# Kernel tuning notes

Hardware: AMD Instinct MI355X
Metric: run time of the kernel (lower is better)

The kernel has to match this reference:

```python
import jax, jax.numpy as jnp
import numpy as np

H = 8  # n_head
EPS = 1e-5


def layernorm(x, g, b):
    m = jnp.mean(x, -1, keepdims=True)
    v = jnp.mean((x - m) ** 2, -1, keepdims=True)
    return (x - m) * jax.lax.rsqrt(v + EPS) * g + b


def setup_inputs() -> dict:
    key = jax.random.key(0)
    ks = jax.random.split(key, 32)
    b, t, d, f, n_mem, l_mem = 4, 256, 512, 2048, 64, 128
    sd = 1.0 / np.sqrt(d)
    sf = 1.0 / np.sqrt(f)
    rn = lambda k, shape, s: jax.random.normal(k, shape, jnp.float32) * s
    inp = {
        'dec_output': rn(ks[0], (b, t, d), 1.0),
        'tgt_mask': jnp.ones((b, t), dtype=bool),
        'mem_attn_out': rn(ks[1], (b, t, n_mem + 1), 1.0),
        'enc_out_mem': rn(ks[2], (n_mem, l_mem, d), 1.0),
        'tgt_emb_mem': rn(ks[3], (n_mem, l_mem, d), 1.0),
        'tgt_mask_mem': jnp.ones((n_mem, l_mem), dtype=bool),
        # MultiHeadedAttention params
        'Wq': rn(ks[4], (d, d), sd), 'bq': jnp.zeros((d,)),
        'Wk': rn(ks[5], (d, d), sd), 'bk': jnp.zeros((d,)),
        'Wv': rn(ks[6], (d, d), sd), 'bv': jnp.zeros((d,)),
        'Wo': rn(ks[7], (d, d), sd), 'bo': jnp.zeros((d,)),
        # LayerNorms (norms[0] pre, norms[1] post)
        'g0': jnp.ones((d,)), 'be0': jnp.zeros((d,)),
        'g1': jnp.ones((d,)), 'be1': jnp.zeros((d,)),
        # pos_ffn (applied to attended tokens)
        'W1': rn(ks[8], (d, f), sd), 'bf1': jnp.zeros((f,)),
        'W2': rn(ks[9], (f, d), sf), 'bf2': jnp.zeros((d,)),
        # pos_ffn2 (applied to all tokens at the end)
        'W3': rn(ks[10], (d, f), sd), 'bf3': jnp.zeros((f,)),
        'W4': rn(ks[11], (f, d), sf), 'bf4': jnp.zeros((d,)),
    }
    return inp


def reference(dec_output, tgt_mask, mem_attn_out, enc_out_mem, tgt_emb_mem, tgt_mask_mem,
              Wq, bq, Wk, bk, Wv, bv, Wo, bo, g0, be0, g1, be1,
              W1, bf1, W2, bf2, W3, bf3, W4, bf4):
    b, t, d = dec_output.shape
    dh = d // H
    x = layernorm(dec_output, g0, be0)                       # norms[0]

    samples = jnp.argmax(mem_attn_out, -1) - 1               # [b,t], -1 => no memory
    valid = samples >= 0
    s = jnp.clip(samples, 0, None)                           # safe gather index

    # Per-token gather of the selected memory entry (irregular access).
    K = enc_out_mem[s]                                       # [b,t,l_mem,d]
    V = tgt_emb_mem[s]                                       # [b,t,l_mem,d]
    kmask = tgt_mask_mem[s]                                  # [b,t,l_mem] True=valid

    # Single-row attention: token (b,t) queries memory entry samples[b,t].
    q = (x @ Wq + bq).reshape(b, t, H, dh)
    k = (K @ Wk + bk).reshape(b, t, -1, H, dh)
    v = (V @ Wv + bv).reshape(b, t, -1, H, dh)
    scores = jnp.einsum('bthd,btlhd->bthl', q, k) / np.sqrt(dh)
    scores = jnp.where(kmask[:, :, None, :], scores, -1e9)
    attn = jax.nn.softmax(scores, axis=-1)
    ctx = jnp.einsum('bthl,btlhd->bthd', attn, v).reshape(b, t, d)
    st = ctx @ Wo + bo + x                                   # residual = query

    # pos_ffn (residual) then norms[1]
    st = st + jax.nn.relu(st @ W1 + bf1) @ W2 + bf2
    st = layernorm(st, g1, be1)

    # scatter-back: zero for tokens with sample == -1
    x = x + jnp.where(valid[..., None], st, 0.0)

    # pos_ffn2 (residual)
    out = x + jax.nn.relu(x @ W3 + bf3) @ W4 + bf4
    return out
```

## Files before the change

kernel.cpp:

```cpp
#include <hip/hip_runtime.h>
#include <hip/hip_bf16.h>
#include <math.h>

#define DD    512
#define FF    2048
#define NMEM  64
#define LMEM  128
#define NH    8
#define DH    64
#define NTOK  1024
#define NMROW 8192

typedef __attribute__((ext_vector_type(4))) float f32x4;
typedef __attribute__((ext_vector_type(8))) short bf16x8;

__device__ inline unsigned short f2b(float f) {
    union { float f; unsigned int i; } u; u.f = f;
    unsigned int r = u.i + 0x7FFFu + ((u.i >> 16) & 1u);
    return (unsigned short)(r >> 16);
}
__device__ inline float b2f(unsigned short b) {
    union { unsigned int i; float f; } u; u.i = ((unsigned int)b) << 16;
    return u.f;
}
__device__ __forceinline__ void gload_lds(const void* src, void* dst) {
    __builtin_amdgcn_global_load_lds((const __attribute__((address_space(1))) void*)src,
        (__attribute__((address_space(3))) void*)dst, 16, 0, 0);
}

struct WSeg { const float* src; unsigned short* dst; int K, N, tile0; };
struct PrepArgs {
    const float4 *enc, *emb; ushort4 *encb, *embb;
    WSeg s[8];
    const float *mem_attn;
    int *samples, *blist, *bstart;
    const float *dec, *g0, *be0;
    float *x; unsigned short *xb, *ctxb;
};

__global__ __launch_bounds__(256)
void prep_kernel(PrepArgs a) {
    __shared__ float ld[32][33];
    __shared__ float red[8];
    __shared__ int ibuf[64 + 65 + 64];
    int b = blockIdx.x, tid = threadIdx.x;
    if (b < 4096) {
        int i = b * 256 + tid;
        float4 va = a.enc[i];
        a.encb[i] = make_ushort4(f2b(va.x), f2b(va.y), f2b(va.z), f2b(va.w));
        float4 vb = a.emb[i];
        a.embb[i] = make_ushort4(f2b(vb.x), f2b(vb.y), f2b(vb.z), f2b(vb.w));
        return;
    }
    if (b < 9216) {
        int t = b - 4096;
        int si = 0;
#pragma unroll
        for (int i = 1; i < 8; ++i) if (t >= a.s[i].tile0) si = i;
        const float* src = a.s[si].src;
        unsigned short* dst = a.s[si].dst;
        int K = a.s[si].K, N = a.s[si].N;
        int lt = t - a.s[si].tile0;
        int ntn = N >> 5;
        int k0 = (lt / ntn) << 5, n0 = (lt % ntn) << 5;
        int r = tid >> 3, c = (tid & 7) << 2;
        float4 v = *(const float4*)(src + (size_t)(k0 + r) * N + n0 + c);
        ld[r][c] = v.x; ld[r][c + 1] = v.y; ld[r][c + 2] = v.z; ld[r][c + 3] = v.w;
        __syncthreads();
        ushort4 o = make_ushort4(f2b(ld[c][r]), f2b(ld[c + 1][r]),
                                 f2b(ld[c + 2][r]), f2b(ld[c + 3][r]));
        *(ushort4*)(dst + (size_t)(n0 + r) * K + k0 + c) = o;
        return;
    }
    if (b < 10240) {
        int row = b - 9216;
        const float* xr = a.dec + (size_t)row * DD;
        float v0 = xr[tid], v1 = xr[tid + 256];
        float s = v0 + v1, s2 = v0 * v0 + v1 * v1;
        for (int off = 32; off > 0; off >>= 1) {
            s  += __shfl_down(s,  off, 64);
            s2 += __shfl_down(s2, off, 64);
        }
        int wave = tid >> 6, lane = tid & 63;
        if (lane == 0) { red[wave] = s; red[4 + wave] = s2; }
        __syncthreads();
        float S  = red[0] + red[1] + red[2] + red[3];
        float S2 = red[4] + red[5] + red[6] + red[7];
        float mean = S / (float)DD;
        float inv  = rsqrtf(S2 / (float)DD - mean * mean + 1e-5f);
        float o0 = (v0 - mean) * inv * a.g0[tid]       + a.be0[tid];
        float o1 = (v1 - mean) * inv * a.g0[tid + 256] + a.be0[tid + 256];
        size_t base = (size_t)row * DD;
        a.x[base + tid] = o0; a.x[base + tid + 256] = o1;
        a.xb[base + tid] = f2b(o0); a.xb[base + tid + 256] = f2b(o1);
        ((unsigned*)a.ctxb)[row * 256 + tid] = 0u;
        return;
    }
    int* scnt  = ibuf;
    int* soff  = ibuf + 64;
    int* scnt2 = ibuf + 129;
    if (tid < 64) { scnt[tid] = 0; scnt2[tid] = 0; }
    __syncthreads();
    int mys[4];
#pragma unroll
    for (int k = 0; k < 4; ++k) {
        int t = k * 256 + tid;
        const float* r = a.mem_attn + (size_t)t * (NMEM + 1);
        float best = r[0]; int bi = 0;
        for (int i = 1; i < NMEM + 1; ++i) {
            float v = r[i];
            if (v > best) { best = v; bi = i; }
        }
        int s = bi - 1;
        a.samples[t] = s; mys[k] = s;
        if (s >= 0) atomicAdd(&scnt[s], 1);
    }
    __syncthreads();
    if (tid == 0) {
        int run = 0;
        for (int e = 0; e < 64; ++e) { soff[e] = run; run += scnt[e]; }
        soff[64] = run;
    }
    __syncthreads();
    if (tid < 65) a.bstart[tid] = soff[tid];
#pragma unroll
    for (int k = 0; k < 4; ++k) {
        int t = k * 256 + tid;
        int s = mys[k];
        if (s >= 0) {
            int pos = soff[s] + atomicAdd(&scnt2[s], 1);
            a.blist[pos] = t;
        }
    }
}

__global__ __launch_bounds__(256)
void ln_scatter_kernel(const float* __restrict__ st2, const float* __restrict__ g,
                       const float* __restrict__ be, const float* __restrict__ x,
                       const int* __restrict__ samples, float* __restrict__ x2,
                       unsigned short* __restrict__ x2b) {
    int row = blockIdx.x;
    const float* xr = st2 + (size_t)row * DD;
    int tid = threadIdx.x;
    float v0 = xr[tid], v1 = xr[tid + 256];
    float s = v0 + v1, s2 = v0 * v0 + v1 * v1;
    for (int off = 32; off > 0; off >>= 1) {
        s  += __shfl_down(s,  off, 64);
        s2 += __shfl_down(s2, off, 64);
    }
    __shared__ float red[8];
    int wave = tid >> 6, lane = tid & 63;
    if (lane == 0) { red[wave] = s; red[4 + wave] = s2; }
    __syncthreads();
    float S  = red[0] + red[1] + red[2] + red[3];
    float S2 = red[4] + red[5] + red[6] + red[7];
    float mean = S / (float)DD;
    float inv  = rsqrtf(S2 / (float)DD - mean * mean + 1e-5f);
    float valid = (samples[row] >= 0) ? 1.f : 0.f;
    size_t base = (size_t)row * DD;
    float l0 = (v0 - mean) * inv * g[tid]       + be[tid];
    float l1 = (v1 - mean) * inv * g[tid + 256] + be[tid + 256];
    float r0 = x[base + tid]       + valid * l0;
    float r1 = x[base + tid + 256] + valid * l1;
    x2[base + tid] = r0; x2[base + tid + 256] = r1;
    x2b[base + tid] = f2b(r0); x2b[base + tid + 256] = f2b(r1);
}

template<int MI, int NI, int BK>
__device__ __forceinline__
void gemm_core(const unsigned short* __restrict__ A, const unsigned short* __restrict__ Bt,
               const float* __restrict__ bias, const float* __restrict__ res,
               float* __restrict__ C, unsigned short* __restrict__ Cb,
               int N, int K, int relu, int bx, int by,
               unsigned short* As0, unsigned short* As1,
               unsigned short* Bs0, unsigned short* Bs1) {
    constexpr int BM = MI * 32, BN = NI * 32;
    constexpr int CPR = BK / 8;
    constexpr int RB  = BK * 2;
    const int tid = threadIdx.x;
    const int lane = tid & 63, w = tid >> 6;
    const int wm = (w >> 1) * (MI * 16), wn = (w & 1) * (NI * 16);
    const int m0 = by * BM, n0 = bx * BN;
    f32x4 acc[MI][NI] = {};

    auto stage = [&](unsigned short* As, unsigned short* Bs, int k0) {
#pragma unroll
        for (int it = 0; it < BM * CPR / 256; ++it) {
            int f = it * 256 + tid;
            int row = f / CPR, ch = f % CPR;
            int sch = ch ^ (row & 7);
            gload_lds((const char*)(A + (size_t)(m0 + row) * K + k0) + sch * 16,
                      (char*)As + f * 16);
        }
#pragma unroll
        for (int it = 0; it < BN * CPR / 256; ++it) {
            int f = it * 256 + tid;
            int row = f / CPR, ch = f % CPR;
            int sch = ch ^ (row & 7);
            gload_lds((const char*)(Bt + (size_t)(n0 + row) * K + k0) + sch * 16,
                      (char*)Bs + f * 16);
        }
    };

    const int nt = K / BK;
    stage(As0, Bs0, 0);
    __syncthreads();
    for (int t = 0; t < nt; ++t) {
        unsigned short* As = (t & 1) ? As1 : As0;
        unsigned short* Bs = (t & 1) ? Bs1 : Bs0;
        if (t + 1 < nt) stage((t & 1) ? As0 : As1, (t & 1) ? Bs0 : Bs1, (t + 1) * BK);
#pragma unroll
        for (int kk = 0; kk < BK / 32; ++kk) {
            bf16x8 af[MI], bfr[NI];
#pragma unroll
            for (int mi = 0; mi < MI; ++mi) {
                int row = wm + mi * 16 + (lane & 15);
                int ch = kk * 4 + (lane >> 4);
                af[mi] = *(const bf16x8*)((const char*)As + row * RB + ((ch ^ (row & 7)) * 16));
            }
#pragma unroll
            for (int ni = 0; ni < NI; ++ni) {
                int row = wn + ni * 16 + (lane & 15);
                int ch = kk * 4 + (lane >> 4);
                bfr[ni] = *(const bf16x8*)((const char*)Bs + row * RB + ((ch ^ (row & 7)) * 16));
            }
#pragma unroll
            for (int mi = 0; mi < MI; ++mi)
#pragma unroll
                for (int ni = 0; ni < NI; ++ni)
                    acc[mi][ni] = __builtin_amdgcn_mfma_f32_16x16x32_bf16(af[mi], bfr[ni], acc[mi][ni], 0, 0, 0);
        }
        __syncthreads();
    }
#pragma unroll
    for (int mi = 0; mi < MI; ++mi) {
#pragma unroll
        for (int ni = 0; ni < NI; ++ni) {
            int col = n0 + wn + ni * 16 + (lane & 15);
            float bv = bias[col];
#pragma unroll
            for (int j = 0; j < 4; ++j) {
                int row = m0 + wm + mi * 16 + (lane >> 4) * 4 + j;
                size_t idx = (size_t)row * N + col;
                float v = acc[mi][ni][j] + bv;
                if (res)  v += res[idx];
                if (relu) v = fmaxf(v, 0.f);
                if (C)  C[idx] = v;
                if (Cb) Cb[idx] = f2b(v);
            }
        }
    }
}

template<int MI, int NI, int BK, int RELU>
__global__ __launch_bounds__(256)
void gemm_kernel(const unsigned short* __restrict__ A, const unsigned short* __restrict__ Bt,
                 const float* __restrict__ bias, const float* __restrict__ res,
                 float* __restrict__ C, unsigned short* __restrict__ Cb, int N, int K) {
    __shared__ __align__(16) unsigned short As0[MI * 32 * BK], As1[MI * 32 * BK];
    __shared__ __align__(16) unsigned short Bs0[NI * 32 * BK], Bs1[NI * 32 * BK];
    gemm_core<MI, NI, BK>(A, Bt, bias, res, C, Cb, N, K, RELU, blockIdx.x, blockIdx.y,
                          As0, As1, Bs0, Bs1);
}

__global__ __launch_bounds__(256)
void attn_fused_kernel(const unsigned short* __restrict__ encb,
                       const unsigned short* __restrict__ embb,
                       const unsigned short* __restrict__ xb,
                       const unsigned short* __restrict__ WkT,
                       const unsigned short* __restrict__ WvT,
                       const unsigned short* __restrict__ WqT,
                       const float* __restrict__ bk, const float* __restrict__ bv,
                       const float* __restrict__ bq,
                       const int* __restrict__ blist, const int* __restrict__ bstart,
                       unsigned short* __restrict__ ctxb) {
    __shared__ __align__(16) unsigned short As[128 * 64];
    __shared__ __align__(16) unsigned short Ws[64 * 64];
    __shared__ __align__(16) unsigned short Ks[128 * 64];
    __shared__ __align__(16) unsigned short Vt[64 * 128];
    __shared__ float qsb[32 * 64];
    __shared__ float ps[2][128];
    __shared__ float red[8];
    __shared__ int toks[32];
    const int b = blockIdx.x, e = b & 63, h = b >> 6, tid = threadIdx.x;
    const int lane = tid & 63, w = tid >> 6;
    const int beg = bstart[e], end = bstart[e + 1];
    if (end <= beg) return;

#pragma unroll 1
    for (int ph = 0; ph < 2; ++ph) {
        const unsigned short* Am = (ph ? embb : encb) + (size_t)e * LMEM * DD;
        const unsigned short* Wm = (ph ? WvT : WkT) + (size_t)h * DH * DD;
        const float* bias = ph ? bv : bk;
        f32x4 acc[2][4] = {};
        for (int k0 = 0; k0 < DD; k0 += 64) {
            __syncthreads();
#pragma unroll
            for (int it = 0; it < 4; ++it) {
                int f = it * 256 + tid;
                int row = f >> 3, ch = f & 7, sch = ch ^ (row & 7);
                gload_lds((const char*)(Am + (size_t)row * DD + k0) + sch * 16,
                          (char*)As + f * 16);
            }
#pragma unroll
            for (int it = 0; it < 2; ++it) {
                int f = it * 256 + tid;
                int row = f >> 3, ch = f & 7, sch = ch ^ (row & 7);
                gload_lds((const char*)(Wm + (size_t)row * DD + k0) + sch * 16,
                          (char*)Ws + f * 16);
            }
            __syncthreads();
#pragma unroll
            for (int kk = 0; kk < 2; ++kk) {
                int ch = kk * 4 + (lane >> 4);
                bf16x8 af[2], bfr[4];
#pragma unroll
                for (int mi = 0; mi < 2; ++mi) {
                    int row = w * 32 + mi * 16 + (lane & 15);
                    af[mi] = *(const bf16x8*)((const char*)As + row * 128 + ((ch ^ (row & 7)) * 16));
                }
#pragma unroll
                for (int ni = 0; ni < 4; ++ni) {
                    int row = ni * 16 + (lane & 15);
                    bfr[ni] = *(const bf16x8*)((const char*)Ws + row * 128 + ((ch ^ (row & 7)) * 16));
                }
#pragma unroll
                for (int mi = 0; mi < 2; ++mi)
#pragma unroll
                    for (int ni = 0; ni < 4; ++ni)
                        acc[mi][ni] = __builtin_amdgcn_mfma_f32_16x16x32_bf16(af[mi], bfr[ni], acc[mi][ni], 0, 0, 0);
            }
        }
#pragma unroll
        for (int mi = 0; mi < 2; ++mi) {
#pragma unroll
            for (int ni = 0; ni < 4; ++ni) {
                int d = ni * 16 + (lane & 15);
                float bvv = bias[h * DH + d];
#pragma unroll
                for (int j = 0; j < 4; ++j) {
                    int l = w * 32 + mi * 16 + (lane >> 4) * 4 + j;
                    unsigned short val = f2b(acc[mi][ni][j] + bvv);
                    if (ph == 0) {
                        int c = d >> 3;
                        *(unsigned short*)((char*)Ks + l * 128 + ((c ^ (l & 7)) * 16) + (d & 7) * 2) = val;
                    } else {
                        int cc = l >> 3;
                        int slot = (cc & 8) | ((cc ^ d) & 7);
                        *(unsigned short*)((char*)Vt + d * 256 + slot * 16 + (l & 7) * 2) = val;
                    }
                }
            }
        }
    }

    const int sub = tid >> 7, lt = tid & 127;
    for (int g0 = beg; g0 < end; g0 += 32) {
        int gcnt = end - g0; if (gcnt > 32) gcnt = 32;
        __syncthreads();
        if (tid < 32) toks[tid] = blist[(g0 + tid < end) ? (g0 + tid) : (end - 1)];
        f32x4 qacc[2] = {};
        for (int k0 = 0; k0 < DD; k0 += 64) {
            __syncthreads();
            {
                int row = tid >> 3, ch = tid & 7, sch = ch ^ (row & 7);
                gload_lds((const char*)(xb + (size_t)toks[row] * DD + k0) + sch * 16,
                          (char*)As + tid * 16);
            }
#pragma unroll
            for (int it = 0; it < 2; ++it) {
                int f = it * 256 + tid;
                int row = f >> 3, ch = f & 7, sch = ch ^ (row & 7);
                gload_lds((const char*)(WqT + (size_t)(h * DH + row) * DD + k0) + sch * 16,
                          (char*)Ws + f * 16);
            }
            __syncthreads();
#pragma unroll
            for (int kk = 0; kk < 2; ++kk) {
                int ch = kk * 4 + (lane >> 4);
                int ar = (w >> 1) * 16 + (lane & 15);
                bf16x8 af = *(const bf16x8*)((const char*)As + ar * 128 + ((ch ^ (ar & 7)) * 16));
#pragma unroll
                for (int ni = 0; ni < 2; ++ni) {
                    int br = (w & 1) * 32 + ni * 16 + (lane & 15);
                    bf16x8 bfr = *(const bf16x8*)((const char*)Ws + br * 128 + ((ch ^ (br & 7)) * 16));
                    qacc[ni] = __builtin_amdgcn_mfma_f32_16x16x32_bf16(af, bfr, qacc[ni], 0, 0, 0);
                }
            }
        }
#pragma unroll
        for (int ni = 0; ni < 2; ++ni)
#pragma unroll
            for (int j = 0; j < 4; ++j) {
                int r = (w >> 1) * 16 + (lane >> 4) * 4 + j;
                int d = (w & 1) * 32 + ni * 16 + (lane & 15);
                qsb[r * 64 + d] = qacc[ni][j] + bq[h * DH + d];
            }
        __syncthreads();

        int iters = (gcnt + 1) >> 1;
        for (int it = 0; it < iters; ++it) {
            int tl = it * 2 + sub;
            float sc = 0.f;
#pragma unroll
            for (int c = 0; c < 8; ++c) {
                bf16x8 kv = *(const bf16x8*)((char*)Ks + lt * 128 + ((c ^ (lt & 7)) * 16));
#pragma unroll
                for (int j = 0; j < 8; ++j) sc = fmaf(qsb[tl * 64 + c * 8 + j], b2f((unsigned short)kv[j]), sc);
            }
            sc *= 0.125f;
            float mx = sc;
            for (int off = 32; off > 0; off >>= 1) mx = fmaxf(mx, __shfl_xor(mx, off, 64));
            if ((tid & 63) == 0) red[tid >> 6] = mx;
            __syncthreads();
            mx = fmaxf(red[sub * 2], red[sub * 2 + 1]);
            float ex = __expf(sc - mx);
            float sm = ex;
            for (int off = 32; off > 0; off >>= 1) sm += __shfl_xor(sm, off, 64);
            if ((tid & 63) == 0) red[4 + (tid >> 6)] = sm;
            __syncthreads();
            sm = red[4 + sub * 2] + red[4 + sub * 2 + 1];
            ps[sub][lt] = ex / sm;
            __syncthreads();
            if (tid < 128) {
                int sub2 = tid >> 6, d = tid & 63;
                int tl2 = it * 2 + sub2;
                if (g0 + tl2 < end) {
                    int tok2 = toks[tl2];
                    float acc2 = 0.f;
#pragma unroll
                    for (int cc = 0; cc < 16; ++cc) {
                        int slot = (cc & 8) | ((cc ^ d) & 7);
                        bf16x8 vv = *(const bf16x8*)((char*)Vt + d * 256 + slot * 16);
#pragma unroll
                        for (int j = 0; j < 8; ++j) acc2 = fmaf(ps[sub2][cc * 8 + j], b2f((unsigned short)vv[j]), acc2);
                    }
                    ctxb[(size_t)tok2 * DD + h * DH + d] = f2b(acc2);
                }
            }
            __syncthreads();
        }
    }
}

extern "C" void kernel_launch(void* const* d_in, const int* in_sizes, int n_in,
                              void* d_out, int out_size, void* d_ws, size_t ws_size,
                              hipStream_t stream) {
    const float* dec      = (const float*)d_in[0];
    const float* mem_attn = (const float*)d_in[2];
    const float* enc_mem  = (const float*)d_in[3];
    const float* emb_mem  = (const float*)d_in[4];
    const float* Wq = (const float*)d_in[6];  const float* bq = (const float*)d_in[7];
    const float* Wk = (const float*)d_in[8];  const float* bk = (const float*)d_in[9];
    const float* Wv = (const float*)d_in[10]; const float* bv = (const float*)d_in[11];
    const float* Wo = (const float*)d_in[12]; const float* bo = (const float*)d_in[13];
    const float* g0 = (const float*)d_in[14]; const float* be0 = (const float*)d_in[15];
    const float* g1 = (const float*)d_in[16]; const float* be1 = (const float*)d_in[17];
    const float* W1 = (const float*)d_in[18]; const float* bf1 = (const float*)d_in[19];
    const float* W2 = (const float*)d_in[20]; const float* bf2 = (const float*)d_in[21];
    const float* W3 = (const float*)d_in[22]; const float* bf3 = (const float*)d_in[23];
    const float* W4 = (const float*)d_in[24]; const float* bf4 = (const float*)d_in[25];
    float* out = (float*)d_out;

    const size_t MB = 1u << 20;
    char* ws = (char*)d_ws;
    unsigned short* encb  = (unsigned short*)(ws + 0 * MB);
    unsigned short* embb  = (unsigned short*)(ws + 8 * MB);
    unsigned short* WqT = (unsigned short*)(ws + 32 * MB);
    unsigned short* WkT = (unsigned short*)(ws + 32 * MB + 512 * 1024);
    unsigned short* WvT = (unsigned short*)(ws + 33 * MB);
    unsigned short* WoT = (unsigned short*)(ws + 33 * MB + 512 * 1024);
    unsigned short* W1T = (unsigned short*)(ws + 34 * MB);
    unsigned short* W2T = (unsigned short*)(ws + 36 * MB);
    unsigned short* W3T = (unsigned short*)(ws + 38 * MB);
    unsigned short* W4T = (unsigned short*)(ws + 40 * MB);
    float*          x    = (float*)(ws + 42 * MB);
    unsigned short* xb   = (unsigned short*)(ws + 44 * MB);
    unsigned short* ctxb = (unsigned short*)(ws + 47 * MB);
    int*         samples = (int*)(ws + 48 * MB);
    int*         blist   = (int*)(ws + 48 * MB + 4096);
    int*         bstart  = (int*)(ws + 48 * MB + 8192);
    float*          st   = (float*)(ws + 0 * MB);
    unsigned short* stb  = (unsigned short*)(ws + 2 * MB);
    unsigned short* h1b  = (unsigned short*)(ws + 3 * MB);
    float*          st2  = (float*)(ws + 8 * MB);
    float*          x2   = (float*)(ws + 10 * MB);
    unsigned short* x2b  = (unsigned short*)(ws + 12 * MB);
    unsigned short* h2b  = (unsigned short*)(ws + 13 * MB);

    PrepArgs pa;
    pa.enc = (const float4*)enc_mem; pa.emb = (const float4*)emb_mem;
    pa.encb = (ushort4*)encb; pa.embb = (ushort4*)embb;
    pa.s[0] = { Wq, WqT, DD, DD,    0 };
    pa.s[1] = { Wk, WkT, DD, DD,  256 };
    pa.s[2] = { Wv, WvT, DD, DD,  512 };
    pa.s[3] = { Wo, WoT, DD, DD,  768 };
    pa.s[4] = { W1, W1T, DD, FF, 1024 };
    pa.s[5] = { W2, W2T, FF, DD, 2048 };
    pa.s[6] = { W3, W3T, DD, FF, 3072 };
    pa.s[7] = { W4, W4T, FF, DD, 4096 };
    pa.mem_attn = mem_attn; pa.samples = samples; pa.blist = blist; pa.bstart = bstart;
    pa.dec = dec; pa.g0 = g0; pa.be0 = be0;
    pa.x = x; pa.xb = xb; pa.ctxb = ctxb;
    prep_kernel<<<10241, 256, 0, stream>>>(pa);
    attn_fused_kernel<<<512, 256, 0, stream>>>(encb, embb, xb, WkT, WvT, WqT,
                                               bk, bv, bq, blist, bstart, ctxb);
    gemm_kernel<1,1,128,0><<<dim3(16, 32), 256, 0, stream>>>(ctxb, WoT, bo, x, st, stb, DD, DD);
    gemm_kernel<2,2,128,1><<<dim3(32, 16), 256, 0, stream>>>(stb, W1T, bf1, nullptr, nullptr, h1b, FF, DD);
    gemm_kernel<1,1,128,0><<<dim3(16, 32), 256, 0, stream>>>(h1b, W2T, bf2, st, st2, nullptr, DD, FF);
    ln_scatter_kernel<<<NTOK, 256, 0, stream>>>(st2, g1, be1, x, samples, x2, x2b);
    gemm_kernel<2,2,128,1><<<dim3(32, 16), 256, 0, stream>>>(x2b, W3T, bf3, nullptr, nullptr, h2b, FF, DD);
    gemm_kernel<1,1,128,0><<<dim3(16, 32), 256, 0, stream>>>(h2b, W4T, bf4, x2, out, nullptr, DD, FF);
}
```

Measured before the change: 122.6 us.

## Double-buffer attention projections, warp-local softmax, and retune GEMM K tiles

The fused attention kernel now stages its K/V and Q projection loads in double-buffered 32-wide K slices, so the next slice loads while the current one is multiplied. It also gives each wavefront its own token for scores, softmax and context, using readlane broadcasts, which removes block-wide barriers and shared reduction buffers. The Wo GEMM becomes a single-stage kernel with K=512 in one tile, and the W2/W4 GEMMs use BK=256. The cost is more synchronisation steps in the projection loops and larger shared-memory use in the retuned GEMMs, which may lower occupancy.

```diff
diff --git a/kernel.cpp b/kernel.cpp
--- a/kernel.cpp
+++ b/kernel.cpp
@@ -263,24 +263,33 @@
                           As0, As1, Bs0, Bs1);
 }
 
+template<int MI, int NI, int BK, int RELU>
 __global__ __launch_bounds__(256)
-void attn_fused_kernel(const unsigned short* __restrict__ encb,
-                       const unsigned short* __restrict__ embb,
-                       const unsigned short* __restrict__ xb,
-                       const unsigned short* __restrict__ WkT,
-                       const unsigned short* __restrict__ WvT,
-                       const unsigned short* __restrict__ WqT,
-                       const float* __restrict__ bk, const float* __restrict__ bv,
-                       const float* __restrict__ bq,
-                       const int* __restrict__ blist, const int* __restrict__ bstart,
-                       unsigned short* __restrict__ ctxb) {
-    __shared__ __align__(16) unsigned short As[128 * 64];
-    __shared__ __align__(16) unsigned short Ws[64 * 64];
+void gemm1_kernel(const unsigned short* __restrict__ A, const unsigned short* __restrict__ Bt,
+                  const float* __restrict__ bias, const float* __restrict__ res,
+                  float* __restrict__ C, unsigned short* __restrict__ Cb, int N) {
+    __shared__ __align__(16) unsigned short As[MI * 32 * BK];
+    __shared__ __align__(16) unsigned short Bs[NI * 32 * BK];
+    gemm_core<MI, NI, BK>(A, Bt, bias, res, C, Cb, N, BK, RELU, blockIdx.x, blockIdx.y,
+                          As, As, Bs, Bs);
+}
+
+__global__ __launch_bounds__(256)
+void attn_fused2_kernel(const unsigned short* __restrict__ encb,
+                        const unsigned short* __restrict__ embb,
+                        const unsigned short* __restrict__ xb,
+                        const unsigned short* __restrict__ WkT,
+                        const unsigned short* __restrict__ WvT,
+                        const unsigned short* __restrict__ WqT,
+                        const float* __restrict__ bk, const float* __restrict__ bv,
+                        const float* __restrict__ bq,
+                        const int* __restrict__ blist, const int* __restrict__ bstart,
+                        unsigned short* __restrict__ ctxb) {
+    __shared__ __align__(16) unsigned short As0[128 * 32], As1[128 * 32];
+    __shared__ __align__(16) unsigned short Ws0[64 * 32],  Ws1[64 * 32];
     __shared__ __align__(16) unsigned short Ks[128 * 64];
     __shared__ __align__(16) unsigned short Vt[64 * 128];
     __shared__ float qsb[32 * 64];
-    __shared__ float ps[2][128];
-    __shared__ float red[8];
     __shared__ int toks[32];
     const int b = blockIdx.x, e = b & 63, h = b >> 6, tid = threadIdx.x;
     const int lane = tid & 63, w = tid >> 6;
@@ -289,47 +298,43 @@
 
 #pragma unroll 1
     for (int ph = 0; ph < 2; ++ph) {
-        const unsigned short* Am = (ph ? embb : encb) + (size_t)e * LMEM * DD;
-        const unsigned short* Wm = (ph ? WvT : WkT) + (size_t)h * DH * DD;
+        const unsigned short* Am = (ph ? embb : encb) + (size_t)e * (LMEM * DD);
+        const unsigned short* Wm = (ph ? WvT : WkT) + (size_t)h * (DH * DD);
         const float* bias = ph ? bv : bk;
         f32x4 acc[2][4] = {};
-        for (int k0 = 0; k0 < DD; k0 += 64) {
+        auto stageP = [&](unsigned short* As, unsigned short* Ws, int k0) {
+#pragma unroll
+            for (int it = 0; it < 2; ++it) {
+                int f = it * 256 + tid, row = f >> 2, ch = f & 3, s = ch ^ (row & 3);
+                gload_lds((const char*)(Am + (size_t)row * DD + k0) + s * 16, (char*)As + f * 16);
+            }
+            { int f = tid, row = f >> 2, ch = f & 3, s = ch ^ (row & 3);
+              gload_lds((const char*)(Wm + (size_t)row * DD + k0) + s * 16, (char*)Ws + f * 16); }
+        };
+        stageP(As0, Ws0, 0);
+        __syncthreads();
+        for (int t = 0; t < 16; ++t) {
+            unsigned short* As = (t & 1) ? As1 : As0;
+            unsigned short* Ws = (t & 1) ? Ws1 : Ws0;
+            if (t + 1 < 16) stageP((t & 1) ? As0 : As1, (t & 1) ? Ws0 : Ws1, (t + 1) * 32);
+            int ch = lane >> 4;
+            bf16x8 af[2], bfr[4];
+#pragma unroll
+            for (int mi = 0; mi < 2; ++mi) {
+                int row = w * 32 + mi * 16 + (lane & 15);
+                af[mi] = *(const bf16x8*)((const char*)As + row * 64 + ((ch ^ (row & 3)) * 16));
+            }
+#pragma unroll
+            for (int ni = 0; ni < 4; ++ni) {
+                int row = ni * 16 + (lane & 15);
+                bfr[ni] = *(const bf16x8*)((const char*)Ws + row * 64 + ((ch ^ (row & 3)) * 16));
+            }
+#pragma unroll
+            for (int mi = 0; mi < 2; ++mi)
+#pragma unroll
+                for (int ni = 0; ni < 4; ++ni)
+                    acc[mi][ni] = __builtin_amdgcn_mfma_f32_16x16x32_bf16(af[mi], bfr[ni], acc[mi][ni], 0, 0, 0);
             __syncthreads();
-#pragma unroll
-            for (int it = 0; it < 4; ++it) {
-                int f = it * 256 + tid;
-                int row = f >> 3, ch = f & 7, sch = ch ^ (row & 7);
-                gload_lds((const char*)(Am + (size_t)row * DD + k0) + sch * 16,
-                          (char*)As + f * 16);
-            }
-#pragma unroll
-            for (int it = 0; it < 2; ++it) {
-                int f = it * 256 + tid;
-                int row = f >> 3, ch = f & 7, sch = ch ^ (row & 7);
-                gload_lds((const char*)(Wm + (size_t)row * DD + k0) + sch * 16,
-                          (char*)Ws + f * 16);
-            }
-            __syncthreads();
-#pragma unroll
-            for (int kk = 0; kk < 2; ++kk) {
-                int ch = kk * 4 + (lane >> 4);
-                bf16x8 af[2], bfr[4];
-#pragma unroll
-                for (int mi = 0; mi < 2; ++mi) {
-                    int row = w * 32 + mi * 16 + (lane & 15);
-                    af[mi] = *(const bf16x8*)((const char*)As + row * 128 + ((ch ^ (row & 7)) * 16));
-                }
-#pragma unroll
-                for (int ni = 0; ni < 4; ++ni) {
-                    int row = ni * 16 + (lane & 15);
-                    bfr[ni] = *(const bf16x8*)((const char*)Ws + row * 128 + ((ch ^ (row & 7)) * 16));
-                }
-#pragma unroll
-                for (int mi = 0; mi < 2; ++mi)
-#pragma unroll
-                    for (int ni = 0; ni < 4; ++ni)
-                        acc[mi][ni] = __builtin_amdgcn_mfma_f32_16x16x32_bf16(af[mi], bfr[ni], acc[mi][ni], 0, 0, 0);
-            }
         }
 #pragma unroll
         for (int mi = 0; mi < 2; ++mi) {
@@ -354,39 +359,38 @@
         }
     }
 
-    const int sub = tid >> 7, lt = tid & 127;
     for (int g0 = beg; g0 < end; g0 += 32) {
         int gcnt = end - g0; if (gcnt > 32) gcnt = 32;
         __syncthreads();
         if (tid < 32) toks[tid] = blist[(g0 + tid < end) ? (g0 + tid) : (end - 1)];
+        __syncthreads();
         f32x4 qacc[2] = {};
-        for (int k0 = 0; k0 < DD; k0 += 64) {
+        auto stageQ = [&](unsigned short* As, unsigned short* Ws, int k0) {
+            if (tid < 128) {
+                int row = tid >> 2, ch = tid & 3, s = ch ^ (row & 3);
+                gload_lds((const char*)(xb + (size_t)toks[row] * DD + k0) + s * 16,
+                          (char*)As + tid * 16);
+            }
+            { int f = tid, row = f >> 2, ch = f & 3, s = ch ^ (row & 3);
+              gload_lds((const char*)(WqT + (size_t)(h * DH + row) * DD + k0) + s * 16,
+                        (char*)Ws + f * 16); }
+        };
+        stageQ(As0, Ws0, 0);
+        __syncthreads();
+        for (int t = 0; t < 16; ++t) {
+            unsigned short* As = (t & 1) ? As1 : As0;
+            unsigned short* Ws = (t & 1) ? Ws1 : Ws0;
+            if (t + 1 < 16) stageQ((t & 1) ? As0 : As1, (t & 1) ? Ws0 : Ws1, (t + 1) * 32);
+            int ch = lane >> 4;
+            int ar = (w >> 1) * 16 + (lane & 15);
+            bf16x8 af = *(const bf16x8*)((const char*)As + ar * 64 + ((ch ^ (ar & 3)) * 16));
+#pragma unroll
+            for (int ni = 0; ni < 2; ++ni) {
+                int br = (w & 1) * 32 + ni * 16 + (lane & 15);
+                bf16x8 bfr = *(const bf16x8*)((const char*)Ws + br * 64 + ((ch ^ (br & 3)) * 16));
+                qacc[ni] = __builtin_amdgcn_mfma_f32_16x16x32_bf16(af, bfr, qacc[ni], 0, 0, 0);
+            }
             __syncthreads();
-            {
-                int row = tid >> 3, ch = tid & 7, sch = ch ^ (row & 7);
-                gload_lds((const char*)(xb + (size_t)toks[row] * DD + k0) + sch * 16,
-                          (char*)As + tid * 16);
-            }
-#pragma unroll
-            for (int it = 0; it < 2; ++it) {
-                int f = it * 256 + tid;
-                int row = f >> 3, ch = f & 7, sch = ch ^ (row & 7);
-                gload_lds((const char*)(WqT + (size_t)(h * DH + row) * DD + k0) + sch * 16,
-                          (char*)Ws + f * 16);
-            }
-            __syncthreads();
-#pragma unroll
-            for (int kk = 0; kk < 2; ++kk) {
-                int ch = kk * 4 + (lane >> 4);
-                int ar = (w >> 1) * 16 + (lane & 15);
-                bf16x8 af = *(const bf16x8*)((const char*)As + ar * 128 + ((ch ^ (ar & 7)) * 16));
-#pragma unroll
-                for (int ni = 0; ni < 2; ++ni) {
-                    int br = (w & 1) * 32 + ni * 16 + (lane & 15);
-                    bf16x8 bfr = *(const bf16x8*)((const char*)Ws + br * 128 + ((ch ^ (br & 7)) * 16));
-                    qacc[ni] = __builtin_amdgcn_mfma_f32_16x16x32_bf16(af, bfr, qacc[ni], 0, 0, 0);
-                }
-            }
         }
 #pragma unroll
         for (int ni = 0; ni < 2; ++ni)
@@ -398,47 +402,44 @@
             }
         __syncthreads();
 
-        int iters = (gcnt + 1) >> 1;
-        for (int it = 0; it < iters; ++it) {
-            int tl = it * 2 + sub;
-            float sc = 0.f;
+        for (int tl = w; tl < gcnt; tl += 4) {
+            int token = toks[tl];
+            float qv = qsb[tl * 64 + lane];
+            int qb = __float_as_int(qv);
+            float sc0 = 0.f, sc1 = 0.f;
 #pragma unroll
             for (int c = 0; c < 8; ++c) {
-                bf16x8 kv = *(const bf16x8*)((char*)Ks + lt * 128 + ((c ^ (lt & 7)) * 16));
-#pragma unroll
-                for (int j = 0; j < 8; ++j) sc = fmaf(qsb[tl * 64 + c * 8 + j], b2f((unsigned short)kv[j]), sc);
-            }
-            sc *= 0.125f;
-            float mx = sc;
+                bf16x8 k0v = *(const bf16x8*)((char*)Ks + lane * 128 + ((c ^ (lane & 7)) * 16));
+                bf16x8 k1v = *(const bf16x8*)((char*)Ks + (lane + 64) * 128 + ((c ^ (lane & 7)) * 16));
+#pragma unroll
+                for (int j = 0; j < 8; ++j) {
+                    float qd = __int_as_float(__builtin_amdgcn_readlane(qb, c * 8 + j));
+                    sc0 = fmaf(qd, b2f((unsigned short)k0v[j]), sc0);
+                    sc1 = fmaf(qd, b2f((unsigned short)k1v[j]), sc1);
+                }
+            }
+            sc0 *= 0.125f; sc1 *= 0.125f;
+            float mx = fmaxf(sc0, sc1);
             for (int off = 32; off > 0; off >>= 1) mx = fmaxf(mx, __shfl_xor(mx, off, 64));
-            if ((tid & 63) == 0) red[tid >> 6] = mx;
-            __syncthreads();
-            mx = fmaxf(red[sub * 2], red[sub * 2 + 1]);
-            float ex = __expf(sc - mx);
-            float sm = ex;
+            float p0 = __expf(sc0 - mx), p1 = __expf(sc1 - mx);
+            float sm = p0 + p1;
             for (int off = 32; off > 0; off >>= 1) sm += __shfl_xor(sm, off, 64);
-            if ((tid & 63) == 0) red[4 + (tid >> 6)] = sm;
-            __syncthreads();
-            sm = red[4 + sub * 2] + red[4 + sub * 2 + 1];
-            ps[sub][lt] = ex / sm;
-            __syncthreads();
-            if (tid < 128) {
-                int sub2 = tid >> 6, d = tid & 63;
-                int tl2 = it * 2 + sub2;
-                if (g0 + tl2 < end) {
-                    int tok2 = toks[tl2];
-                    float acc2 = 0.f;
-#pragma unroll
-                    for (int cc = 0; cc < 16; ++cc) {
-                        int slot = (cc & 8) | ((cc ^ d) & 7);
-                        bf16x8 vv = *(const bf16x8*)((char*)Vt + d * 256 + slot * 16);
-#pragma unroll
-                        for (int j = 0; j < 8; ++j) acc2 = fmaf(ps[sub2][cc * 8 + j], b2f((unsigned short)vv[j]), acc2);
-                    }
-                    ctxb[(size_t)tok2 * DD + h * DH + d] = f2b(acc2);
+            float inv = 1.f / sm;
+            int p0b = __float_as_int(p0 * inv), p1b = __float_as_int(p1 * inv);
+            float acc2 = 0.f;
+            const int d = lane;
+#pragma unroll
+            for (int cc = 0; cc < 16; ++cc) {
+                int slot = (cc & 8) | ((cc ^ d) & 7);
+                bf16x8 vv = *(const bf16x8*)((char*)Vt + d * 256 + slot * 16);
+#pragma unroll
+                for (int j = 0; j < 8; ++j) {
+                    int l = cc * 8 + j;
+                    float pl = __int_as_float(__builtin_amdgcn_readlane(l < 64 ? p0b : p1b, l & 63));
+                    acc2 = fmaf(pl, b2f((unsigned short)vv[j]), acc2);
                 }
             }
-            __syncthreads();
+            ctxb[(size_t)token * DD + h * DH + d] = f2b(acc2);
         }
     }
 }
@@ -503,12 +504,12 @@
     pa.dec = dec; pa.g0 = g0; pa.be0 = be0;
     pa.x = x; pa.xb = xb; pa.ctxb = ctxb;
     prep_kernel<<<10241, 256, 0, stream>>>(pa);
-    attn_fused_kernel<<<512, 256, 0, stream>>>(encb, embb, xb, WkT, WvT, WqT,
-                                               bk, bv, bq, blist, bstart, ctxb);
-    gemm_kernel<1,1,128,0><<<dim3(16, 32), 256, 0, stream>>>(ctxb, WoT, bo, x, st, stb, DD, DD);
+    attn_fused2_kernel<<<512, 256, 0, stream>>>(encb, embb, xb, WkT, WvT, WqT,
+                                                bk, bv, bq, blist, bstart, ctxb);
+    gemm1_kernel<1,1,512,0><<<dim3(16, 32), 256, 0, stream>>>(ctxb, WoT, bo, x, st, stb, DD);
     gemm_kernel<2,2,128,1><<<dim3(32, 16), 256, 0, stream>>>(stb, W1T, bf1, nullptr, nullptr, h1b, FF, DD);
-    gemm_kernel<1,1,128,0><<<dim3(16, 32), 256, 0, stream>>>(h1b, W2T, bf2, st, st2, nullptr, DD, FF);
+    gemm_kernel<1,1,256,0><<<dim3(16, 32), 256, 0, stream>>>(h1b, W2T, bf2, st, st2, nullptr, DD, FF);
     ln_scatter_kernel<<<NTOK, 256, 0, stream>>>(st2, g1, be1, x, samples, x2, x2b);
     gemm_kernel<2,2,128,1><<<dim3(32, 16), 256, 0, stream>>>(x2b, W3T, bf3, nullptr, nullptr, h2b, FF, DD);
-    gemm_kernel<1,1,128,0><<<dim3(16, 32), 256, 0, stream>>>(h2b, W4T, bf4, x2, out, nullptr, DD, FF);
-}
+    gemm_kernel<1,1,256,0><<<dim3(16, 32), 256, 0, stream>>>(h2b, W4T, bf4, x2, out, nullptr, DD, FF);
+}
```

After: 132.5 us. 1.08x slower.

## Overlap weight transposes with attention and deepen GEMM prefetch pipeline

Applied to the files above, without the earlier changes.

Moves the transpose/bf16 conversion of Wo, W1-W4 out of the prep kernel into extra blocks of the attention kernel, so that work runs alongside attention blocks instead of in a separate serial stage. The GEMM core now prefetches two tiles ahead, using explicit vmcnt waits and raw barriers in place of full syncthreads. The Wo GEMM gets a single-stage full-K variant, and the W2/W4 GEMMs use BK=256. This adds hand-tuned waitcnt assumptions (8 loads per thread per tile) and larger LDS footprints, which may lower occupancy.

```diff
diff --git a/kernel.cpp b/kernel.cpp
--- a/kernel.cpp
+++ b/kernel.cpp
@@ -29,9 +29,10 @@
 }
 
 struct WSeg { const float* src; unsigned short* dst; int K, N, tile0; };
+
 struct PrepArgs {
     const float4 *enc, *emb; ushort4 *encb, *embb;
-    WSeg s[8];
+    WSeg s[3];
     const float *mem_attn;
     int *samples, *blist, *bstart;
     const float *dec, *g0, *be0;
@@ -52,11 +53,11 @@
         a.embb[i] = make_ushort4(f2b(vb.x), f2b(vb.y), f2b(vb.z), f2b(vb.w));
         return;
     }
-    if (b < 9216) {
+    if (b < 4864) {
         int t = b - 4096;
         int si = 0;
 #pragma unroll
-        for (int i = 1; i < 8; ++i) if (t >= a.s[i].tile0) si = i;
+        for (int i = 1; i < 3; ++i) if (t >= a.s[i].tile0) si = i;
         const float* src = a.s[si].src;
         unsigned short* dst = a.s[si].dst;
         int K = a.s[si].K, N = a.s[si].N;
@@ -72,8 +73,8 @@
         *(ushort4*)(dst + (size_t)(n0 + r) * K + k0 + c) = o;
         return;
     }
-    if (b < 10240) {
-        int row = b - 9216;
+    if (b < 5888) {
+        int row = b - 4864;
         const float* xr = a.dec + (size_t)row * DD;
         float v0 = xr[tid], v1 = xr[tid + 256];
         float s = v0 + v1, s2 = v0 * v0 + v1 * v1;
@@ -177,6 +178,7 @@
     constexpr int BM = MI * 32, BN = NI * 32;
     constexpr int CPR = BK / 8;
     constexpr int RB  = BK * 2;
+    static_assert((BM * CPR + BN * CPR) / 256 == 8 || BK == 512, "8 loads/wave/tile");
     const int tid = threadIdx.x;
     const int lane = tid & 63, w = tid >> 6;
     const int wm = (w >> 1) * (MI * 16), wn = (w & 1) * (NI * 16);
@@ -204,11 +206,17 @@
 
     const int nt = K / BK;
     stage(As0, Bs0, 0);
-    __syncthreads();
+    if (nt > 1) stage(As1, Bs1, BK);
     for (int t = 0; t < nt; ++t) {
-        unsigned short* As = (t & 1) ? As1 : As0;
-        unsigned short* Bs = (t & 1) ? Bs1 : Bs0;
-        if (t + 1 < nt) stage((t & 1) ? As0 : As1, (t & 1) ? Bs0 : Bs1, (t + 1) * BK);
+        if (t + 1 < nt) {
+            asm volatile("s_waitcnt vmcnt(8)" ::: "memory");
+        } else {
+            asm volatile("s_waitcnt vmcnt(0)" ::: "memory");
+        }
+        __builtin_amdgcn_s_barrier();
+        __builtin_amdgcn_sched_barrier(0);
+        const unsigned short* As = (t & 1) ? As1 : As0;
+        const unsigned short* Bs = (t & 1) ? Bs1 : Bs0;
 #pragma unroll
         for (int kk = 0; kk < BK / 32; ++kk) {
             bf16x8 af[MI], bfr[NI];
@@ -230,7 +238,9 @@
                 for (int ni = 0; ni < NI; ++ni)
                     acc[mi][ni] = __builtin_amdgcn_mfma_f32_16x16x32_bf16(af[mi], bfr[ni], acc[mi][ni], 0, 0, 0);
         }
-        __syncthreads();
+        __builtin_amdgcn_s_barrier();
+        if (t + 2 < nt)
+            stage((t & 1) ? As1 : As0, (t & 1) ? Bs1 : Bs0, (t + 2) * BK);
     }
 #pragma unroll
     for (int mi = 0; mi < MI; ++mi) {
@@ -262,6 +272,19 @@
     gemm_core<MI, NI, BK>(A, Bt, bias, res, C, Cb, N, K, RELU, blockIdx.x, blockIdx.y,
                           As0, As1, Bs0, Bs1);
 }
+
+template<int MI, int NI, int BK, int RELU>
+__global__ __launch_bounds__(256)
+void gemm1_kernel(const unsigned short* __restrict__ A, const unsigned short* __restrict__ Bt,
+                  const float* __restrict__ bias, const float* __restrict__ res,
+                  float* __restrict__ C, unsigned short* __restrict__ Cb, int N) {
+    __shared__ __align__(16) unsigned short As[MI * 32 * BK];
+    __shared__ __align__(16) unsigned short Bs[NI * 32 * BK];
+    gemm_core<MI, NI, BK>(A, Bt, bias, res, C, Cb, N, BK, RELU, blockIdx.x, blockIdx.y,
+                          As, As, Bs, Bs);
+}
+
+struct WSeg5s { WSeg s[5]; };
 
 __global__ __launch_bounds__(256)
 void attn_fused_kernel(const unsigned short* __restrict__ encb,
@@ -273,7 +296,7 @@
                        const float* __restrict__ bk, const float* __restrict__ bv,
                        const float* __restrict__ bq,
                        const int* __restrict__ blist, const int* __restrict__ bstart,
-                       unsigned short* __restrict__ ctxb) {
+                       unsigned short* __restrict__ ctxb, WSeg5s wsegs) {
     __shared__ __align__(16) unsigned short As[128 * 64];
     __shared__ __align__(16) unsigned short Ws[64 * 64];
     __shared__ __align__(16) unsigned short Ks[128 * 64];
@@ -282,8 +305,37 @@
     __shared__ float ps[2][128];
     __shared__ float red[8];
     __shared__ int toks[32];
-    const int b = blockIdx.x, e = b & 63, h = b >> 6, tid = threadIdx.x;
+    const int b = blockIdx.x, tid = threadIdx.x;
     const int lane = tid & 63, w = tid >> 6;
+
+    if (b >= 512) {
+        float* ld = (float*)As;
+#pragma unroll 1
+        for (int j = 0; j < 8; ++j) {
+            int t = (b - 512) * 8 + j;
+            int si = 0;
+#pragma unroll
+            for (int i = 1; i < 5; ++i) if (t >= wsegs.s[i].tile0) si = i;
+            const float* src = wsegs.s[si].src;
+            unsigned short* dst = wsegs.s[si].dst;
+            int K = wsegs.s[si].K, N = wsegs.s[si].N;
+            int lt = t - wsegs.s[si].tile0;
+            int ntn = N >> 5;
+            int k0 = (lt / ntn) << 5, n0 = (lt % ntn) << 5;
+            int r = tid >> 3, c = (tid & 7) << 2;
+            float4 v = *(const float4*)(src + (size_t)(k0 + r) * N + n0 + c);
+            ld[r * 33 + c] = v.x; ld[r * 33 + c + 1] = v.y;
+            ld[r * 33 + c + 2] = v.z; ld[r * 33 + c + 3] = v.w;
+            __syncthreads();
+            ushort4 o = make_ushort4(f2b(ld[c * 33 + r]), f2b(ld[(c + 1) * 33 + r]),
+                                     f2b(ld[(c + 2) * 33 + r]), f2b(ld[(c + 3) * 33 + r]));
+            *(ushort4*)(dst + (size_t)(n0 + r) * K + k0 + c) = o;
+            __syncthreads();
+        }
+        return;
+    }
+
+    const int e = b & 63, h = b >> 6;
     const int beg = bstart[e], end = bstart[e + 1];
     if (end <= beg) return;
 
@@ -491,24 +543,25 @@
     PrepArgs pa;
     pa.enc = (const float4*)enc_mem; pa.emb = (const float4*)emb_mem;
     pa.encb = (ushort4*)encb; pa.embb = (ushort4*)embb;
-    pa.s[0] = { Wq, WqT, DD, DD,    0 };
-    pa.s[1] = { Wk, WkT, DD, DD,  256 };
-    pa.s[2] = { Wv, WvT, DD, DD,  512 };
-    pa.s[3] = { Wo, WoT, DD, DD,  768 };
-    pa.s[4] = { W1, W1T, DD, FF, 1024 };
-    pa.s[5] = { W2, W2T, FF, DD, 2048 };
-    pa.s[6] = { W3, W3T, DD, FF, 3072 };
-    pa.s[7] = { W4, W4T, FF, DD, 4096 };
+    pa.s[0] = { Wq, WqT, DD, DD,   0 };
+    pa.s[1] = { Wk, WkT, DD, DD, 256 };
+    pa.s[2] = { Wv, WvT, DD, DD, 512 };
     pa.mem_attn = mem_attn; pa.samples = samples; pa.blist = blist; pa.bstart = bstart;
     pa.dec = dec; pa.g0 = g0; pa.be0 = be0;
     pa.x = x; pa.xb = xb; pa.ctxb = ctxb;
-    prep_kernel<<<10241, 256, 0, stream>>>(pa);
-    attn_fused_kernel<<<512, 256, 0, stream>>>(encb, embb, xb, WkT, WvT, WqT,
-                                               bk, bv, bq, blist, bstart, ctxb);
-    gemm_kernel<1,1,128,0><<<dim3(16, 32), 256, 0, stream>>>(ctxb, WoT, bo, x, st, stb, DD, DD);
+    prep_kernel<<<5889, 256, 0, stream>>>(pa);
+    WSeg5s wt;
+    wt.s[0] = { Wo, WoT, DD, DD,    0 };
+    wt.s[1] = { W1, W1T, DD, FF,  256 };
+    wt.s[2] = { W2, W2T, FF, DD, 1280 };
+    wt.s[3] = { W3, W3T, DD, FF, 2304 };
+    wt.s[4] = { W4, W4T, FF, DD, 3328 };
+    attn_fused_kernel<<<512 + 544, 256, 0, stream>>>(encb, embb, xb, WkT, WvT, WqT,
+                                                     bk, bv, bq, blist, bstart, ctxb, wt);
+    gemm1_kernel<1,1,512,0><<<dim3(16, 32), 256, 0, stream>>>(ctxb, WoT, bo, x, st, stb, DD);
     gemm_kernel<2,2,128,1><<<dim3(32, 16), 256, 0, stream>>>(stb, W1T, bf1, nullptr, nullptr, h1b, FF, DD);
-    gemm_kernel<1,1,128,0><<<dim3(16, 32), 256, 0, stream>>>(h1b, W2T, bf2, st, st2, nullptr, DD, FF);
+    gemm_kernel<1,1,256,0><<<dim3(16, 32), 256, 0, stream>>>(h1b, W2T, bf2, st, st2, nullptr, DD, FF);
     ln_scatter_kernel<<<NTOK, 256, 0, stream>>>(st2, g1, be1, x, samples, x2, x2b);
     gemm_kernel<2,2,128,1><<<dim3(32, 16), 256, 0, stream>>>(x2b, W3T, bf3, nullptr, nullptr, h2b, FF, DD);
-    gemm_kernel<1,1,128,0><<<dim3(16, 32), 256, 0, stream>>>(h2b, W4T, bf4, x2, out, nullptr, DD, FF);
-}
+    gemm_kernel<1,1,256,0><<<dim3(16, 32), 256, 0, stream>>>(h2b, W4T, bf4, x2, out, nullptr, DD, FF);
+}
```

Result: no change. 122.4 us, median of 4 (-0.2%).

## Deepen GEMM prefetch pipeline, enlarge K tiles, stream attention K/V operands directly

Applied to the files above, without the earlier changes.

The shared GEMM core now keeps two K-tiles in flight. It waits on the vector-memory counter with explicit s_waitcnt and raw barriers instead of a full __syncthreads before every tile. The Wo projection uses a new single-tile variant with BK=512, and the W2/W4 GEMMs move to BK=256 so there are fewer loop iterations and barriers. The attention kernel's K/V projection now reads operands straight from global memory into registers, skipping the LDS staging and its barriers, and MFMA sections are wrapped in s_setprio. The risks are higher LDS use per block, which can lower occupancy, and uncoalesced or cache-dependent global loads in the attention projection.

```diff
diff --git a/kernel.cpp b/kernel.cpp
--- a/kernel.cpp
+++ b/kernel.cpp
@@ -29,6 +29,7 @@
 }
 
 struct WSeg { const float* src; unsigned short* dst; int K, N, tile0; };
+
 struct PrepArgs {
     const float4 *enc, *emb; ushort4 *encb, *embb;
     WSeg s[8];
@@ -177,6 +178,7 @@
     constexpr int BM = MI * 32, BN = NI * 32;
     constexpr int CPR = BK / 8;
     constexpr int RB  = BK * 2;
+    static_assert((BM * CPR + BN * CPR) / 256 == 8 || BK == 512, "8 loads/wave/tile");
     const int tid = threadIdx.x;
     const int lane = tid & 63, w = tid >> 6;
     const int wm = (w >> 1) * (MI * 16), wn = (w & 1) * (NI * 16);
@@ -204,11 +206,17 @@
 
     const int nt = K / BK;
     stage(As0, Bs0, 0);
-    __syncthreads();
+    if (nt > 1) stage(As1, Bs1, BK);
     for (int t = 0; t < nt; ++t) {
-        unsigned short* As = (t & 1) ? As1 : As0;
-        unsigned short* Bs = (t & 1) ? Bs1 : Bs0;
-        if (t + 1 < nt) stage((t & 1) ? As0 : As1, (t & 1) ? Bs0 : Bs1, (t + 1) * BK);
+        if (t + 1 < nt) {
+            asm volatile("s_waitcnt vmcnt(8)" ::: "memory");
+        } else {
+            asm volatile("s_waitcnt vmcnt(0)" ::: "memory");
+        }
+        __builtin_amdgcn_s_barrier();
+        __builtin_amdgcn_sched_barrier(0);
+        const unsigned short* As = (t & 1) ? As1 : As0;
+        const unsigned short* Bs = (t & 1) ? Bs1 : Bs0;
 #pragma unroll
         for (int kk = 0; kk < BK / 32; ++kk) {
             bf16x8 af[MI], bfr[NI];
@@ -230,7 +238,9 @@
                 for (int ni = 0; ni < NI; ++ni)
                     acc[mi][ni] = __builtin_amdgcn_mfma_f32_16x16x32_bf16(af[mi], bfr[ni], acc[mi][ni], 0, 0, 0);
         }
-        __syncthreads();
+        __builtin_amdgcn_s_barrier();
+        if (t + 2 < nt)
+            stage((t & 1) ? As1 : As0, (t & 1) ? Bs1 : Bs0, (t + 2) * BK);
     }
 #pragma unroll
     for (int mi = 0; mi < MI; ++mi) {
@@ -261,6 +271,17 @@
     __shared__ __align__(16) unsigned short Bs0[NI * 32 * BK], Bs1[NI * 32 * BK];
     gemm_core<MI, NI, BK>(A, Bt, bias, res, C, Cb, N, K, RELU, blockIdx.x, blockIdx.y,
                           As0, As1, Bs0, Bs1);
+}
+
+template<int MI, int NI, int BK, int RELU>
+__global__ __launch_bounds__(256)
+void gemm1_kernel(const unsigned short* __restrict__ A, const unsigned short* __restrict__ Bt,
+                  const float* __restrict__ bias, const float* __restrict__ res,
+                  float* __restrict__ C, unsigned short* __restrict__ Cb, int N) {
+    __shared__ __align__(16) unsigned short As[MI * 32 * BK];
+    __shared__ __align__(16) unsigned short Bs[NI * 32 * BK];
+    gemm_core<MI, NI, BK>(A, Bt, bias, res, C, Cb, N, BK, RELU, blockIdx.x, blockIdx.y,
+                          As, As, Bs, Bs);
 }
 
 __global__ __launch_bounds__(256)
@@ -282,54 +303,35 @@
     __shared__ float ps[2][128];
     __shared__ float red[8];
     __shared__ int toks[32];
-    const int b = blockIdx.x, e = b & 63, h = b >> 6, tid = threadIdx.x;
+    const int b = blockIdx.x, tid = threadIdx.x;
     const int lane = tid & 63, w = tid >> 6;
+    const int e = b & 63, h = b >> 6;
     const int beg = bstart[e], end = bstart[e + 1];
     if (end <= beg) return;
 
 #pragma unroll 1
     for (int ph = 0; ph < 2; ++ph) {
-        const unsigned short* Am = (ph ? embb : encb) + (size_t)e * LMEM * DD;
-        const unsigned short* Wm = (ph ? WvT : WkT) + (size_t)h * DH * DD;
+        const unsigned short* Am = (ph ? embb : encb) + (size_t)e * (LMEM * DD);
+        const unsigned short* Wm = (ph ? WvT : WkT) + (size_t)h * (DH * DD);
         const float* bias = ph ? bv : bk;
         f32x4 acc[2][4] = {};
-        for (int k0 = 0; k0 < DD; k0 += 64) {
-            __syncthreads();
-#pragma unroll
-            for (int it = 0; it < 4; ++it) {
-                int f = it * 256 + tid;
-                int row = f >> 3, ch = f & 7, sch = ch ^ (row & 7);
-                gload_lds((const char*)(Am + (size_t)row * DD + k0) + sch * 16,
-                          (char*)As + f * 16);
-            }
-#pragma unroll
-            for (int it = 0; it < 2; ++it) {
-                int f = it * 256 + tid;
-                int row = f >> 3, ch = f & 7, sch = ch ^ (row & 7);
-                gload_lds((const char*)(Wm + (size_t)row * DD + k0) + sch * 16,
-                          (char*)Ws + f * 16);
-            }
-            __syncthreads();
-#pragma unroll
-            for (int kk = 0; kk < 2; ++kk) {
-                int ch = kk * 4 + (lane >> 4);
-                bf16x8 af[2], bfr[4];
-#pragma unroll
-                for (int mi = 0; mi < 2; ++mi) {
-                    int row = w * 32 + mi * 16 + (lane & 15);
-                    af[mi] = *(const bf16x8*)((const char*)As + row * 128 + ((ch ^ (row & 7)) * 16));
-                }
-#pragma unroll
-                for (int ni = 0; ni < 4; ++ni) {
-                    int row = ni * 16 + (lane & 15);
-                    bfr[ni] = *(const bf16x8*)((const char*)Ws + row * 128 + ((ch ^ (row & 7)) * 16));
-                }
-#pragma unroll
-                for (int mi = 0; mi < 2; ++mi)
-#pragma unroll
-                    for (int ni = 0; ni < 4; ++ni)
-                        acc[mi][ni] = __builtin_amdgcn_mfma_f32_16x16x32_bf16(af[mi], bfr[ni], acc[mi][ni], 0, 0, 0);
-            }
+        const unsigned short* ar0 = Am + (size_t)(w * 32 + (lane & 15)) * DD + (lane >> 4) * 8;
+        const unsigned short* br0 = Wm + (size_t)(lane & 15) * DD + (lane >> 4) * 8;
+#pragma unroll 4
+        for (int ks = 0; ks < 16; ++ks) {
+            bf16x8 af[2], bfr[4];
+            af[0] = *(const bf16x8*)(ar0 + ks * 32);
+            af[1] = *(const bf16x8*)(ar0 + 16 * DD + ks * 32);
+#pragma unroll
+            for (int ni = 0; ni < 4; ++ni)
+                bfr[ni] = *(const bf16x8*)(br0 + (size_t)ni * 16 * DD + ks * 32);
+            __builtin_amdgcn_s_setprio(1);
+#pragma unroll
+            for (int mi = 0; mi < 2; ++mi)
+#pragma unroll
+                for (int ni = 0; ni < 4; ++ni)
+                    acc[mi][ni] = __builtin_amdgcn_mfma_f32_16x16x32_bf16(af[mi], bfr[ni], acc[mi][ni], 0, 0, 0);
+            __builtin_amdgcn_s_setprio(0);
         }
 #pragma unroll
         for (int mi = 0; mi < 2; ++mi) {
@@ -353,6 +355,7 @@
             }
         }
     }
+    __syncthreads();
 
     const int sub = tid >> 7, lt = tid & 127;
     for (int g0 = beg; g0 < end; g0 += 32) {
@@ -375,6 +378,7 @@
                           (char*)Ws + f * 16);
             }
             __syncthreads();
+            __builtin_amdgcn_s_setprio(1);
 #pragma unroll
             for (int kk = 0; kk < 2; ++kk) {
                 int ch = kk * 4 + (lane >> 4);
@@ -387,6 +391,7 @@
                     qacc[ni] = __builtin_amdgcn_mfma_f32_16x16x32_bf16(af, bfr, qacc[ni], 0, 0, 0);
                 }
             }
+            __builtin_amdgcn_s_setprio(0);
         }
 #pragma unroll
         for (int ni = 0; ni < 2; ++ni)
@@ -505,10 +510,10 @@
     prep_kernel<<<10241, 256, 0, stream>>>(pa);
     attn_fused_kernel<<<512, 256, 0, stream>>>(encb, embb, xb, WkT, WvT, WqT,
                                                bk, bv, bq, blist, bstart, ctxb);
-    gemm_kernel<1,1,128,0><<<dim3(16, 32), 256, 0, stream>>>(ctxb, WoT, bo, x, st, stb, DD, DD);
+    gemm1_kernel<1,1,512,0><<<dim3(16, 32), 256, 0, stream>>>(ctxb, WoT, bo, x, st, stb, DD);
     gemm_kernel<2,2,128,1><<<dim3(32, 16), 256, 0, stream>>>(stb, W1T, bf1, nullptr, nullptr, h1b, FF, DD);
-    gemm_kernel<1,1,128,0><<<dim3(16, 32), 256, 0, stream>>>(h1b, W2T, bf2, st, st2, nullptr, DD, FF);
+    gemm_kernel<1,1,256,0><<<dim3(16, 32), 256, 0, stream>>>(h1b, W2T, bf2, st, st2, nullptr, DD, FF);
     ln_scatter_kernel<<<NTOK, 256, 0, stream>>>(st2, g1, be1, x, samples, x2, x2b);
     gemm_kernel<2,2,128,1><<<dim3(32, 16), 256, 0, stream>>>(x2b, W3T, bf3, nullptr, nullptr, h2b, FF, DD);
-    gemm_kernel<1,1,128,0><<<dim3(16, 32), 256, 0, stream>>>(h2b, W4T, bf4, x2, out, nullptr, DD, FF);
-}
+    gemm_kernel<1,1,256,0><<<dim3(16, 32), 256, 0, stream>>>(h2b, W4T, bf4, x2, out, nullptr, DD, FF);
+}
```

Result: slower. 150.2 us (+22.5%).
